# Optimization experiments

Measured on AMD Instinct MI355X. Metric: run time of the kernel, lower is better.

Reference implementation:

```python
import jax, jax.numpy as jnp
import numpy as np
import math

V, D, H, NH, LE, LD = 32000, 256, 1024, 8, 2, 2
B, T = 4, 512


def qlinear(x, W, b):
    # x: [..., Din, 4]; W: [4, Dout, Din] (r,i,j,k); b: [Dout, 4] or None
    r, i, j, k = x[..., 0], x[..., 1], x[..., 2], x[..., 3]
    Wr, Wi, Wj, Wk = W[0], W[1], W[2], W[3]
    f = lambda a, M: jnp.einsum('...d,od->...o', a, M)
    ro = f(r, Wr) - f(i, Wi) - f(j, Wj) - f(k, Wk)
    io = f(r, Wi) + f(i, Wr) + f(j, Wk) - f(k, Wj)
    jo = f(r, Wj) - f(i, Wk) + f(j, Wr) + f(k, Wi)
    ko = f(r, Wk) + f(i, Wj) - f(j, Wi) + f(k, Wr)
    out = jnp.stack([ro, io, jo, ko], axis=-1)
    return out + b if b is not None else out


def modrelu(x, bias):
    # x: [..., F, 4]; bias: [F]
    norm = jnp.linalg.norm(x, axis=-1)
    scale = jax.nn.relu(norm + bias) / (norm + 1e-6)
    return x * scale[..., None]


def qnorm(x, g, beta):
    # normalize each quaternion (last dim of size 4) to unit norm
    n = jnp.sqrt(jnp.sum(x * x, axis=-1, keepdims=True) + 1e-6)
    return g * (x / n) + beta


def qattn(q, k, v, W, b, mask, nh):
    # W: [4(proj q,k,v,out), 4(comp), D, D]; b: [4, D, 4]
    def split(x):
        Bq, Tq, Dq, _ = x.shape
        return x.reshape(Bq, Tq, nh, Dq // nh, 4).transpose(0, 2, 1, 3, 4)
    qh = split(qlinear(q, W[0], b[0]))
    kh = split(qlinear(k, W[1], b[1]))
    vh = split(qlinear(v, W[2], b[2]))
    hd = qh.shape[3]
    s = jnp.einsum('bhqfd,bhkfd->bhqk', qh, kh) / math.sqrt(hd * 4)
    if mask is not None:
        s = jnp.where(mask[:, None] == 0, -jnp.inf, s)
    w = jax.nn.softmax(s, axis=-1)
    o = jnp.einsum('bhqk,bhkfd->bhqfd', w, vh)
    Bq, h, Tq, f, _ = o.shape
    o = o.transpose(0, 2, 1, 3, 4).reshape(Bq, Tq, h * f, 4)
    return qlinear(o, W[3], b[3])


def qff(x, W1, b1, mbias, W2, b2):
    return qlinear(modrelu(qlinear(x, W1, b1), mbias), W2, b2)


def qembed(ids, emb):
    d = emb.shape[-1]
    scale = 1.0 / 10000.0 ** (jnp.arange(d, dtype=jnp.float32) / d)
    r = emb[0][ids]
    i = emb[1][ids] * scale
    j = emb[2][ids] * scale
    k = emb[3][ids] * scale
    n = jnp.sqrt(r * r + i * i + j * j + k * k + 1e-6)
    return jnp.stack([r / n, i / n, j / n, k / n], axis=-1)


def rope(x):
    t, d = x.shape[1], x.shape[2]
    inv = 1.0 / 10000.0 ** (jnp.arange(0, d, 2, dtype=jnp.float32) / d)
    fr = jnp.arange(t, dtype=jnp.float32)[:, None] * inv[None, :]
    ang = jnp.concatenate([jnp.sin(fr), jnp.cos(fr)], axis=-1)  # [T, D]
    return x * ang[None, :, :, None]


def setup_inputs():
    key = jax.random.key(0)
    ks = jax.random.split(key, 12)
    n = lambda k, s: jax.random.normal(k, s, jnp.float32) * 0.02
    src = jax.random.randint(ks[0], (B, T), 0, V)
    tgt = jax.random.randint(ks[1], (B, T), 0, V)
    tgt_mask = jnp.broadcast_to(jnp.tril(jnp.ones((T, T), jnp.int32)), (B, T, T))
    return dict(
        src=src, tgt=tgt, tgt_mask=tgt_mask,
        emb=n(ks[2], (4, V, D)),
        enc_attn_W=n(ks[3], (LE, 4, 4, D, D)), enc_attn_b=jnp.zeros((LE, 4, D, 4)),
        enc_norm_g=jnp.ones((LE, 2, D, 4)), enc_norm_b=jnp.zeros((LE, 2, D, 4)),
        enc_ff_W1=n(ks[4], (LE, 4, H, D)), enc_ff_b1=jnp.zeros((LE, H, 4)),
        enc_ff_mod=jnp.zeros((LE, H)),
        enc_ff_W2=n(ks[5], (LE, 4, D, H)), enc_ff_b2=jnp.zeros((LE, D, 4)),
        dec_sa_W=n(ks[6], (LD, 4, 4, D, D)), dec_sa_b=jnp.zeros((LD, 4, D, 4)),
        dec_ca_W=n(ks[7], (LD, 4, 4, D, D)), dec_ca_b=jnp.zeros((LD, 4, D, 4)),
        dec_norm_g=jnp.ones((LD, 3, D, 4)), dec_norm_b=jnp.zeros((LD, 3, D, 4)),
        dec_ff_W1=n(ks[8], (LD, 4, H, D)), dec_ff_b1=jnp.zeros((LD, H, 4)),
        dec_ff_mod=jnp.zeros((LD, H)),
        dec_ff_W2=n(ks[9], (LD, 4, D, H)), dec_ff_b2=jnp.zeros((LD, D, 4)),
        fc_W=n(ks[10], (V, D)), fc_b=jnp.zeros((V,)),
    )


def reference(src, tgt, tgt_mask, emb,
              enc_attn_W, enc_attn_b, enc_norm_g, enc_norm_b,
              enc_ff_W1, enc_ff_b1, enc_ff_mod, enc_ff_W2, enc_ff_b2,
              dec_sa_W, dec_sa_b, dec_ca_W, dec_ca_b, dec_norm_g, dec_norm_b,
              dec_ff_W1, dec_ff_b1, dec_ff_mod, dec_ff_W2, dec_ff_b2,
              fc_W, fc_b):
    x_src = rope(qembed(src, emb))
    x_tgt = rope(qembed(tgt, emb))
    # encoder stack
    m = x_src
    for l in range(LE):
        m = qnorm(m + qattn(m, m, m, enc_attn_W[l], enc_attn_b[l], None, NH), enc_norm_g[l, 0], enc_norm_b[l, 0])
        m = qnorm(m + qff(m, enc_ff_W1[l], enc_ff_b1[l], enc_ff_mod[l], enc_ff_W2[l], enc_ff_b2[l]), enc_norm_g[l, 1], enc_norm_b[l, 1])
    # decoder stack
    x = x_tgt
    for l in range(LD):
        x = qnorm(x + qattn(x, x, x, dec_sa_W[l], dec_sa_b[l], tgt_mask, NH), dec_norm_g[l, 0], dec_norm_b[l, 0])
        x = qnorm(x + qattn(x, m, m, dec_ca_W[l], dec_ca_b[l], None, NH), dec_norm_g[l, 1], dec_norm_b[l, 1])
        x = qnorm(x + qff(x, dec_ff_W1[l], dec_ff_b1[l], dec_ff_mod[l], dec_ff_W2[l], dec_ff_b2[l]), dec_norm_g[l, 2], dec_norm_b[l, 2])
    real = jnp.linalg.norm(x, axis=-1)  # QuaternionToReal('norm') -> [B, T, D]
    logits = jnp.einsum('btd,vd->btv', real, fc_W) + fc_b
    return logits
```

## Files before the change

### kernel.cpp

```cpp
#include <hip/hip_runtime.h>
#include <math.h>

#define B 4
#define T 512
#define D 256
#define H 1024
#define NH 8
#define V 32000
#define BT (B*T)
#define LE 2
#define LD 2
#define DIM 1024

typedef __attribute__((ext_vector_type(8))) short s16x8;
typedef __attribute__((ext_vector_type(4))) float f32x4;
typedef __attribute__((address_space(3))) void lds_void;
typedef const __attribute__((address_space(1))) void g_void;

__device__ __forceinline__ ushort f2bf(float x) {
  uint u = __float_as_uint(x);
  return (ushort)((u + 0x7fffu + ((u >> 16) & 1u)) >> 16);
}

#define QSCALE 0.08838834764831845f

#define A_CNT  1572864
#define F_CNT  2097152
#define FC_CNT 2048000
#define EMB_CNT (2 * BT * 256)
#define MEGA_TOT (A_CNT + F_CNT + FC_CNT + EMB_CNT)
#define WSTEP  1048576
#define FFW    4194304

__device__ __forceinline__ void qexpand_write(
    const float* __restrict__ src, ushort* __restrict__ dst,
    int o, int d, int Din, int P) {
  float w0 = src[(size_t)o * Din + d];
  float w1 = src[P + (size_t)o * Din + d];
  float w2 = src[2 * (size_t)P + (size_t)o * Din + d];
  float w3 = src[3 * (size_t)P + (size_t)o * Din + d];
  int K4 = Din * 4;
  size_t rbase = (size_t)(o * 4) * K4 + d * 4;
  *(ushort4*)(dst + rbase)          = make_ushort4(f2bf(w0), f2bf(-w1), f2bf(-w2), f2bf(-w3));
  *(ushort4*)(dst + rbase + K4)     = make_ushort4(f2bf(w1), f2bf(w0),  f2bf(w3),  f2bf(-w2));
  *(ushort4*)(dst + rbase + 2 * K4) = make_ushort4(f2bf(w2), f2bf(-w3), f2bf(w0),  f2bf(w1));
  *(ushort4*)(dst + rbase + 3 * K4) = make_ushort4(f2bf(w3), f2bf(w2),  f2bf(-w1), f2bf(w0));
}

__global__ __launch_bounds__(256) void mega_expand_kernel(
    const float* __restrict__ encA, const float* __restrict__ decSA,
    const float* __restrict__ decCA,
    const float* __restrict__ eW1, const float* __restrict__ eW2,
    const float* __restrict__ dW1, const float* __restrict__ dW2,
    const float* __restrict__ fcW,
    ushort* __restrict__ WA, ushort* __restrict__ WF, ushort* __restrict__ Wfc,
    const int* __restrict__ srcIds, const int* __restrict__ tgtIds,
    const float* __restrict__ emb,
    float* __restrict__ xsrc, ushort* __restrict__ xbfs,
    float* __restrict__ xtgt, ushort* __restrict__ xbft) {
  int gid = blockIdx.x * 256 + threadIdx.x;
  if (gid < A_CNT) {
    int u = gid >> 18;
    int p = (gid >> 16) & 3;
    int rem = gid & 65535;
    int o = rem >> 8, d = rem & 255;
    const float* base = (u < 2) ? encA + (size_t)u * 1048576
                      : (u < 4) ? decSA + (size_t)(u - 2) * 1048576
                                : decCA + (size_t)(u - 4) * 1048576;
    qexpand_write(base + (size_t)p * 262144,
                  WA + ((size_t)u * 4 + p) * WSTEP, o, d, 256, 65536);
  } else if (gid < A_CNT + F_CNT) {
    int idx = gid - A_CNT;
    int layer = idx >> 19;
    int w12 = (idx >> 18) & 1;
    int rem = idx & 262143;
    const float* w1b = (layer < 2) ? eW1 + (size_t)layer * 1048576
                                   : dW1 + (size_t)(layer - 2) * 1048576;
    const float* w2b = (layer < 2) ? eW2 + (size_t)layer * 1048576
                                   : dW2 + (size_t)(layer - 2) * 1048576;
    ushort* dst = WF + (size_t)layer * 2 * FFW + (size_t)w12 * FFW;
    if (w12 == 0) {
      int o = rem >> 8, d = rem & 255;
      qexpand_write(w1b, dst, o, d, 256, 262144);
    } else {
      int o = rem >> 10, d = rem & 1023;
      qexpand_write(w2b, dst, o, d, 1024, 262144);
    }
  } else if (gid < A_CNT + F_CNT + FC_CNT) {
    int idx = gid - A_CNT - F_CNT;
    float4 v = ((const float4*)fcW)[idx];
    ((ushort4*)Wfc)[idx] = make_ushort4(f2bf(v.x), f2bf(v.y), f2bf(v.z), f2bf(v.w));
  } else if (gid < MEGA_TOT) {
    int idx = gid - A_CNT - F_CNT - FC_CNT;
    int g = idx >> 8, d = idx & 255;
    int isTgt = g >= BT;
    int bt = isTgt ? g - BT : g;
    int id = isTgt ? tgtIds[bt] : srcIds[bt];
    float* out = isTgt ? xtgt : xsrc;
    ushort* outbf = isTgt ? xbft : xbfs;
    int t = bt % T;
    size_t VD = (size_t)V * D;
    float scale = powf(10000.f, -(float)d / (float)D);
    float r = emb[(size_t)id * D + d];
    float i = emb[VD + (size_t)id * D + d] * scale;
    float j = emb[2 * VD + (size_t)id * D + d] * scale;
    float k = emb[3 * VD + (size_t)id * D + d] * scale;
    float n = sqrtf(r * r + i * i + j * j + k * k + 1e-6f);
    float ang;
    if (d < D / 2) {
      float inv = powf(10000.f, -(float)(2 * d) / (float)D);
      ang = sinf((float)t * inv);
    } else {
      float inv = powf(10000.f, -(float)(2 * (d - D / 2)) / (float)D);
      ang = cosf((float)t * inv);
    }
    float s = ang / n;
    size_t base = (size_t)bt * DIM + d * 4;
    float4 q = make_float4(r * s, i * s, j * s, k * s);
    *(float4*)(out + base) = q;
    *(ushort4*)(outbf + base) = make_ushort4(f2bf(q.x), f2bf(q.y), f2bf(q.z), f2bf(q.w));
  }
}

struct GP {
  const ushort* A; const ushort* Aalt; int altStart;
  const ushort* Bt; const float* bias; void* Cv;
  ushort* qo; ushort* ko; ushort* vo;
  float* xres; ushort* xbf; const float* gg; const float* bb;
  const float* modb; ushort* realout;
};

template <int OMODE, int TM>
__global__ __launch_bounds__(256, 4) void gemm_bf16_kernel(
    GP u0, GP u1, int nunits, int N, int K) {
  constexpr int NBUF = (TM == 64) ? 4 : 2;
  __shared__ ushort As[NBUF][TM * 32];
  __shared__ ushort Bs[NBUF][128 * 32];
  const int tid = threadIdx.x;
  const int w = tid >> 6, l = tid & 63;
  const int nwg = gridDim.x;
  const int qq = nwg >> 3, rr = nwg & 7;
  const int xcd = blockIdx.x & 7, pos = blockIdx.x >> 3;
  const int wg = (xcd < rr ? xcd * (qq + 1) : rr * (qq + 1) + (xcd - rr) * qq) + pos;
  const int uwg = nwg / nunits;
  const int unit = wg / uwg;
  const int wgl = wg - unit * uwg;
  GP U = unit ? u1 : u0;
  const int nbx = N >> 7;
  const int nby = uwg / nbx;
  const int m0 = (wgl % nby) * TM, n0 = (wgl / nby) * 128;
  const ushort* Ap = (U.altStart && n0 >= U.altStart) ? U.Aalt : U.A;
  const ushort* Btp = U.Bt;
  const int lr = l & 15, lg = l >> 4;
  constexpr int NR = (TM == 128) ? 4 : 2;
  const int wm = (TM == 128) ? (w >> 1) : 0;
  const int wn = (TM == 128) ? (w & 1) : w;
  const int wcol = wn * (NR * 16);
  f32x4 acc[4][NR] = {};
  const int NT = K >> 5;

  auto stage = [&](int t, int buf) {
    int k0 = t << 5;
#pragma unroll
    for (int s = 0; s < TM / 64; ++s) {
      int fb = (w * (TM / 64) + s) * 1024;
      int f = fb + l * 16;
      int row = f >> 6, cb = (f & 63) >> 1;
      __builtin_amdgcn_global_load_lds(
          (g_void*)(Ap + (size_t)(m0 + row) * K + k0 + cb),
          (lds_void*)((char*)&As[buf][0] + fb), 16, 0, 0);
    }
#pragma unroll
    for (int s = 0; s < 2; ++s) {
      int fb = (w * 2 + s) * 1024;
      int f = fb + l * 16;
      int row = f >> 6, cb = (f & 63) >> 1;
      __builtin_amdgcn_global_load_lds(
          (g_void*)(Btp + (size_t)(n0 + row) * K + k0 + cb),
          (lds_void*)((char*)&Bs[buf][0] + fb), 16, 0, 0);
    }
  };
  auto compute = [&](int buf) {
    s16x8 af[4], bfr[NR];
#pragma unroll
    for (int mi = 0; mi < 4; ++mi)
      af[mi] = *(const s16x8*)(&As[buf][0] + (wm * 64 + mi * 16 + lr) * 32 + lg * 8);
#pragma unroll
    for (int ni = 0; ni < NR; ++ni)
      bfr[ni] = *(const s16x8*)(&Bs[buf][0] + (wcol + ni * 16 + lr) * 32 + lg * 8);
    __builtin_amdgcn_s_setprio(1);
#pragma unroll
    for (int mi = 0; mi < 4; ++mi)
#pragma unroll
      for (int ni = 0; ni < NR; ++ni)
        acc[mi][ni] = __builtin_amdgcn_mfma_f32_16x16x32_bf16(af[mi], bfr[ni], acc[mi][ni], 0, 0, 0);
    __builtin_amdgcn_s_setprio(0);
  };

  if constexpr (TM == 64) {
    stage(0, 0);
    stage(1, 1);
    __syncthreads();
    for (int t = 0; t < NT; t += 2) {
      if (t + 2 < NT) {
        stage(t + 2, (t + 2) & 3);
        stage(t + 3, (t + 3) & 3);
      }
      compute(t & 3);
      compute((t + 1) & 3);
      __syncthreads();
    }
  } else {
    stage(0, 0);
    __syncthreads();
    int cur = 0;
    for (int t = 0; t < NT; ++t) {
      if (t + 1 < NT) stage(t + 1, cur ^ 1);
      compute(cur);
      __syncthreads();
      cur ^= 1;
    }
  }

#pragma unroll
  for (int mi = 0; mi < 4; ++mi) {
#pragma unroll
    for (int ni = 0; ni < NR; ++ni) {
      int row = m0 + wm * 64 + mi * 16 + lg * 4;
      int col = n0 + wcol + ni * 16 + lr;
      f32x4 v = acc[mi][ni];
      if constexpr (OMODE == 0) {
        float bv = U.bias ? U.bias[col] : 0.f;
        float* C = (float*)U.Cv;
#pragma unroll
        for (int r = 0; r < 4; ++r)
          C[(size_t)(row + r) * N + col] = v[r] + bv;
      } else if constexpr (OMODE == 3) {
        float bv = U.bias[col];
        if (col < 2048) {
          ushort* dst = (col < DIM) ? U.qo : U.ko;
          float sc = (col < DIM) ? QSCALE : 1.f;
          int c = col & (DIM - 1);
#pragma unroll
          for (int r = 0; r < 4; ++r)
            dst[(size_t)(row + r) * DIM + c] = f2bf((v[r] + bv) * sc);
        } else {
          int c = col - 2048;
          ushort4 o4 = make_ushort4(f2bf(v[0] + bv), f2bf(v[1] + bv),
                                    f2bf(v[2] + bv), f2bf(v[3] + bv));
          *(ushort4*)&U.vo[((size_t)((row >> 9) << 10) + c) * T + (row & 511)] = o4;
        }
      } else if constexpr (OMODE == 4) {
        float bv = U.bias[col];
        float gv = U.gg[col], bev = U.bb[col];
#pragma unroll
        for (int r = 0; r < 4; ++r) {
          float val = v[r] + bv + U.xres[(size_t)(row + r) * DIM + col];
          float sq = val * val;
          sq += __shfl_xor(sq, 1);
          sq += __shfl_xor(sq, 2);
          float invn = rsqrtf(sq + 1e-6f);
          float res = gv * (val * invn) + bev;
          U.xres[(size_t)(row + r) * DIM + col] = res;
          U.xbf[(size_t)(row + r) * DIM + col] = f2bf(res);
          if (U.realout) {
            float rsq = res * res;
            rsq += __shfl_xor(rsq, 1);
            rsq += __shfl_xor(rsq, 2);
            if ((col & 3) == 0)
              U.realout[(size_t)(row + r) * D + (col >> 2)] = f2bf(sqrtf(rsq));
          }
        }
      } else {
        float bv = U.bias[col];
        float mb = U.modb[col >> 2];
        ushort* C = (ushort*)U.Cv;
#pragma unroll
        for (int r = 0; r < 4; ++r) {
          float val = v[r] + bv;
          float sq = val * val;
          sq += __shfl_xor(sq, 1);
          sq += __shfl_xor(sq, 2);
          float norm = sqrtf(sq);
          float scale = fmaxf(norm + mb, 0.f) / (norm + 1e-6f);
          C[(size_t)(row + r) * N + col] = f2bf(val * scale);
        }
      }
    }
  }
}

__global__ __launch_bounds__(256) void fused_attn_kernel(
    const ushort* __restrict__ qb, const ushort* __restrict__ kb,
    const ushort* __restrict__ vT, ushort* __restrict__ outA,
    int c0, int c1) {
  __shared__ ushort Ks[2][64 * 128];
  __shared__ ushort Vs[2][128 * 64];
  __shared__ ushort Pst[4][1024];
  const int tid = threadIdx.x;
  const int wq = tid >> 6, l = tid & 63;
  const int lr = l & 15, lg = l >> 4;
  const int h = blockIdx.y;
  const int u = blockIdx.z >> 2, b = blockIdx.z & 3;
  const size_t uoff = (size_t)u * ((size_t)BT * DIM);
  const int causal = u ? c1 : c0;
  const int q0 = blockIdx.x * 64 + wq * 16;
  const size_t bT = (size_t)b * T;
  const int hc = h * 128;
  const size_t vrow0 = (size_t)(b * NH + h) * 128;
  const ushort* qbu = qb + uoff;
  const ushort* kbu = kb + uoff;
  const ushort* vTu = vT + uoff;
  ushort* outu = outA + uoff;
  s16x8 qf[4];
#pragma unroll
  for (int ks = 0; ks < 4; ++ks)
    qf[ks] = *(const s16x8*)(qbu + (bT + q0 + lr) * DIM + hc + ks * 32 + lg * 8);
  f32x4 O[8] = {};
  float m[4] = {-3e38f, -3e38f, -3e38f, -3e38f};
  float lac[4] = {0.f, 0.f, 0.f, 0.f};
  const int kend = causal ? (blockIdx.x + 1) * 64 : T;
  const int ntile = kend >> 6;

  auto stageKV = [&](int tile, int buf) {
    int kv0 = tile << 6;
#pragma unroll
    for (int s = 0; s < 4; ++s) {
      int f = s * 4096 + tid * 16;
      int row = f >> 8, g = (f >> 4) & 15;
      int gs = g ^ (row & 7);
      __builtin_amdgcn_global_load_lds(
          (g_void*)(kbu + (bT + kv0 + row) * DIM + hc + gs * 8),
          (lds_void*)((char*)&Ks[buf][0] + f), 16, 0, 0);
    }
#pragma unroll
    for (int s = 0; s < 4; ++s) {
      int f = s * 4096 + tid * 16;
      int row = f >> 7, g = (f >> 4) & 7;
      int gs = g ^ (row & 7);
      __builtin_amdgcn_global_load_lds(
          (g_void*)(vTu + (vrow0 + row) * T + kv0 + gs * 8),
          (lds_void*)((char*)&Vs[buf][0] + f), 16, 0, 0);
    }
  };

  stageKV(0, 0);
  __syncthreads();
  int cur = 0;
  for (int tile = 0; tile < ntile; ++tile) {
    const int kv0 = tile << 6;
    if (tile + 1 < ntile) stageKV(tile + 1, cur ^ 1);
    f32x4 s[4] = {};
#pragma unroll
    for (int ks = 0; ks < 4; ++ks) {
      s16x8 kf[4];
#pragma unroll
      for (int ni = 0; ni < 4; ++ni) {
        int row = ni * 16 + lr;
        int g = (ks * 4 + lg) ^ (row & 7);
        kf[ni] = *(const s16x8*)(&Ks[cur][0] + row * 128 + g * 8);
      }
#pragma unroll
      for (int ni = 0; ni < 4; ++ni)
        s[ni] = __builtin_amdgcn_mfma_f32_16x16x32_bf16(qf[ks], kf[ni], s[ni], 0, 0, 0);
    }
    const bool domask = causal && (kv0 + 63 > q0);
#pragma unroll
    for (int r = 0; r < 4; ++r) {
      const int qrow = q0 + lg * 4 + r;
      float mx = -3e38f;
#pragma unroll
      for (int ni = 0; ni < 4; ++ni) {
        float v = s[ni][r];
        if (domask && (kv0 + ni * 16 + lr > qrow)) v = -3e38f;
        s[ni][r] = v;
        mx = fmaxf(mx, v);
      }
#pragma unroll
      for (int dd = 1; dd < 16; dd <<= 1) mx = fmaxf(mx, __shfl_xor(mx, dd));
      if (__ballot(mx > m[r] + 8.f)) {
        float mn = fmaxf(m[r], mx);
        float alpha = __expf(m[r] - mn);
        m[r] = mn;
        lac[r] *= alpha;
#pragma unroll
        for (int dni = 0; dni < 8; ++dni) O[dni][r] *= alpha;
      }
      float ps = 0.f;
#pragma unroll
      for (int ni = 0; ni < 4; ++ni) {
        float p = __expf(s[ni][r] - m[r]);
        s[ni][r] = p;
        ps += p;
      }
#pragma unroll
      for (int dd = 1; dd < 16; dd <<= 1) ps += __shfl_xor(ps, dd);
      lac[r] += ps;
      const int qloc = lg * 4 + r;
      const int sw = (qloc & 7) << 3;
#pragma unroll
      for (int ni = 0; ni < 4; ++ni)
        Pst[wq][qloc * 64 + ((ni * 16 + lr) ^ sw)] = f2bf(s[ni][r]);
    }
    asm volatile("s_waitcnt lgkmcnt(0)" ::: "memory");
    __builtin_amdgcn_sched_barrier(0);
#pragma unroll
    for (int ks2 = 0; ks2 < 2; ++ks2) {
      s16x8 pa = *(const s16x8*)&Pst[wq][lr * 64 + ((ks2 * 32 + lg * 8) ^ ((lr & 7) << 3))];
#pragma unroll
      for (int dni = 0; dni < 8; ++dni) {
        int row = dni * 16 + lr;
        int g = (ks2 * 4 + lg) ^ (row & 7);
        s16x8 vf = *(const s16x8*)(&Vs[cur][0] + row * 64 + g * 8);
        O[dni] = __builtin_amdgcn_mfma_f32_16x16x32_bf16(pa, vf, O[dni], 0, 0, 0);
      }
    }
    __syncthreads();
    cur ^= 1;
  }
#pragma unroll
  for (int r = 0; r < 4; ++r) {
    float inv = 1.f / lac[r];
    const size_t row = bT + q0 + lg * 4 + r;
#pragma unroll
    for (int dni = 0; dni < 8; ++dni)
      outu[row * DIM + hc + dni * 16 + lr] = f2bf(O[dni][r] * inv);
  }
}

extern "C" void kernel_launch(void* const* d_in, const int* in_sizes, int n_in,
                              void* d_out, int out_size, void* d_ws, size_t ws_size,
                              hipStream_t stream) {
  const int*   src        = (const int*)d_in[0];
  const int*   tgt        = (const int*)d_in[1];
  const float* emb        = (const float*)d_in[3];
  const float* enc_attn_W = (const float*)d_in[4];
  const float* enc_attn_b = (const float*)d_in[5];
  const float* enc_norm_g = (const float*)d_in[6];
  const float* enc_norm_b = (const float*)d_in[7];
  const float* enc_ff_W1  = (const float*)d_in[8];
  const float* enc_ff_b1  = (const float*)d_in[9];
  const float* enc_ff_mod = (const float*)d_in[10];
  const float* enc_ff_W2  = (const float*)d_in[11];
  const float* enc_ff_b2  = (const float*)d_in[12];
  const float* dec_sa_W   = (const float*)d_in[13];
  const float* dec_sa_b   = (const float*)d_in[14];
  const float* dec_ca_W   = (const float*)d_in[15];
  const float* dec_ca_b   = (const float*)d_in[16];
  const float* dec_norm_g = (const float*)d_in[17];
  const float* dec_norm_b = (const float*)d_in[18];
  const float* dec_ff_W1  = (const float*)d_in[19];
  const float* dec_ff_b1  = (const float*)d_in[20];
  const float* dec_ff_mod = (const float*)d_in[21];
  const float* dec_ff_W2  = (const float*)d_in[22];
  const float* dec_ff_b2  = (const float*)d_in[23];
  const float* fc_W       = (const float*)d_in[24];
  const float* fc_b       = (const float*)d_in[25];
  float* out = (float*)d_out;

  const size_t USZ = (size_t)BT * DIM;
  float* ws    = (float*)d_ws;
  float* xsrc  = ws;
  float* xtgt  = xsrc + USZ;
  ushort* xbf_src = (ushort*)(xtgt + USZ);
  ushort* xbf_tgt = xbf_src + USZ;
  ushort* aobf    = xbf_tgt + USZ;
  ushort* qb      = aobf + 2 * USZ;
  ushort* kb      = qb + 2 * USZ;
  ushort* vTb     = kb + 2 * USZ;
  ushort* hbf     = vTb + 2 * USZ;
  ushort* realbf  = hbf + (size_t)BT * H * 4;
  ushort* WA      = realbf + (size_t)BT * D;
  ushort* WF      = WA + (size_t)6 * 4 * WSTEP;
  ushort* Wfc     = WF + (size_t)4 * 2 * FFW;

  mega_expand_kernel<<<(MEGA_TOT + 255) / 256, 256, 0, stream>>>(
      enc_attn_W, dec_sa_W, dec_ca_W,
      enc_ff_W1, enc_ff_W2, dec_ff_W1, dec_ff_W2, fc_W, WA, WF, Wfc,
      src, tgt, emb, xsrc, xbf_src, xtgt, xbf_tgt);

  GP Z{};

  auto mkQKV = [&](const ushort* Abf, const ushort* Wu, const float* bb, int u) {
    GP g = Z;
    g.A = Abf; g.Bt = Wu; g.bias = bb;
    g.qo = qb + u * USZ; g.ko = kb + u * USZ; g.vo = vTb + u * USZ;
    return g;
  };
  auto mkOP = [&](int u, const ushort* Wu3, const float* bb, float* xres,
                  ushort* xbf, const float* gg, const float* nb, ushort* realo) {
    GP g = Z;
    g.A = aobf + u * USZ; g.Bt = Wu3; g.bias = bb;
    g.xres = xres; g.xbf = xbf; g.gg = gg; g.bb = nb; g.realout = realo;
    return g;
  };

  auto qkv1 = [&](GP g) {
    gemm_bf16_kernel<3, 128><<<384, 256, 0, stream>>>(g, g, 1, 3 * DIM, DIM);
  };
  auto qkv2 = [&](GP g0, GP g1) {
    gemm_bf16_kernel<3, 128><<<768, 256, 0, stream>>>(g0, g1, 2, 3 * DIM, DIM);
  };
  auto op1 = [&](GP g) {
    gemm_bf16_kernel<4, 64><<<256, 256, 0, stream>>>(g, g, 1, DIM, DIM);
  };
  auto op2 = [&](GP g0, GP g1) {
    gemm_bf16_kernel<4, 64><<<512, 256, 0, stream>>>(g0, g1, 2, DIM, DIM);
  };
  auto attn1 = [&](int causal) {
    fused_attn_kernel<<<dim3(T / 64, NH, B), 256, 0, stream>>>(
        qb, kb, vTb, aobf, causal, causal);
  };
  auto ffpair = [&](const ushort* xbf, int layer, const float* b1,
                    const float* mod, const float* b2, float* xres,
                    ushort* xbfo, const float* gg, const float* nb,
                    ushort* realo) {
    const ushort* Wf = WF + (size_t)layer * 2 * FFW;
    GP g1 = Z;
    g1.A = xbf; g1.Bt = Wf; g1.bias = b1; g1.Cv = hbf; g1.modb = mod;
    gemm_bf16_kernel<5, 128><<<512, 256, 0, stream>>>(g1, g1, 1, 4 * H, DIM);
    GP g2 = Z;
    g2.A = hbf; g2.Bt = Wf + FFW; g2.bias = b2;
    g2.xres = xres; g2.xbf = xbfo; g2.gg = gg; g2.bb = nb; g2.realout = realo;
    gemm_bf16_kernel<4, 64><<<256, 256, 0, stream>>>(g2, g2, 1, DIM, 4 * H);
  };

  {
    GP e = mkQKV(xbf_src, WA + (size_t)(0 * 4) * WSTEP, enc_attn_b, 0);
    GP d = mkQKV(xbf_tgt, WA + (size_t)(2 * 4) * WSTEP, dec_sa_b, 1);
    qkv2(e, d);
    fused_attn_kernel<<<dim3(T / 64, NH, 2 * B), 256, 0, stream>>>(
        qb, kb, vTb, aobf, 0, 1);
    GP eo = mkOP(0, WA + (size_t)(0 * 4 + 3) * WSTEP, enc_attn_b + 3 * DIM,
                 xsrc, xbf_src, enc_norm_g, enc_norm_b, nullptr);
    GP dd = mkOP(1, WA + (size_t)(2 * 4 + 3) * WSTEP, dec_sa_b + 3 * DIM,
                 xtgt, xbf_tgt, dec_norm_g, dec_norm_b, nullptr);
    op2(eo, dd);
  }
  ffpair(xbf_src, 0, enc_ff_b1, enc_ff_mod, enc_ff_b2, xsrc, xbf_src,
         enc_norm_g + 1 * DIM, enc_norm_b + 1 * DIM, nullptr);
  {
    GP e = mkQKV(xbf_src, WA + (size_t)(1 * 4) * WSTEP,
                 enc_attn_b + (size_t)1 * 4 * DIM, 0);
    qkv1(e);
    attn1(0);
    GP eo = mkOP(0, WA + (size_t)(1 * 4 + 3) * WSTEP,
                 enc_attn_b + (size_t)1 * 4 * DIM + 3 * DIM,
                 xsrc, xbf_src, enc_norm_g + 2 * DIM, enc_norm_b + 2 * DIM, nullptr);
    op1(eo);
  }
  ffpair(xbf_src, 1, enc_ff_b1 + (size_t)1 * H * 4, enc_ff_mod + H,
         enc_ff_b2 + DIM, xsrc, xbf_src,
         enc_norm_g + 3 * DIM, enc_norm_b + 3 * DIM, nullptr);

  for (int l = 0; l < LD; ++l) {
    if (l > 0) {
      GP d = mkQKV(xbf_tgt, WA + (size_t)((2 + l) * 4) * WSTEP,
                   dec_sa_b + (size_t)l * 4 * DIM, 0);
      qkv1(d);
      attn1(1);
      GP od = mkOP(0, WA + (size_t)((2 + l) * 4 + 3) * WSTEP,
                   dec_sa_b + (size_t)l * 4 * DIM + 3 * DIM,
                   xtgt, xbf_tgt, dec_norm_g + (size_t)(l * 3) * DIM,
                   dec_norm_b + (size_t)(l * 3) * DIM, nullptr);
      op1(od);
    }
    {
      GP g = mkQKV(xbf_tgt, WA + (size_t)((4 + l) * 4) * WSTEP,
                   dec_ca_b + (size_t)l * 4 * DIM, 0);
      g.Aalt = xbf_src; g.altStart = DIM;
      qkv1(g);
      attn1(0);
      GP og = mkOP(0, WA + (size_t)((4 + l) * 4 + 3) * WSTEP,
                   dec_ca_b + (size_t)l * 4 * DIM + 3 * DIM,
                   xtgt, xbf_tgt, dec_norm_g + (size_t)(l * 3 + 1) * DIM,
                   dec_norm_b + (size_t)(l * 3 + 1) * DIM, nullptr);
      op1(og);
    }
    ffpair(xbf_tgt, 2 + l, dec_ff_b1 + (size_t)l * H * 4,
           dec_ff_mod + (size_t)l * H, dec_ff_b2 + (size_t)l * DIM,
           xtgt, xbf_tgt, dec_norm_g + (size_t)(l * 3 + 2) * DIM,
           dec_norm_b + (size_t)(l * 3 + 2) * DIM,
           (l == LD - 1) ? realbf : nullptr);
  }

  {
    GP g = Z;
    g.A = realbf; g.Bt = Wfc; g.bias = fc_b; g.Cv = out;
    gemm_bf16_kernel<0, 128><<<(V / 128) * (BT / 128), 256, 0, stream>>>(
        g, g, 1, V, 256);
  }
}
```

Before: 1.092 ms.

## Split-K the FF2 GEMM into four partials with a separate merge kernel

The second feed-forward GEMM (K=4096, N=1024) now runs as a 4-way split-K launch with 1024 workgroups instead of 256. Each split writes bf16 partial sums to a workspace buffer. A new merge kernel sums the partials and applies the bias, residual add, quaternion norm and the optional real-norm output. The aim is better CU occupancy for the long-K GEMM, paid for with an extra kernel launch, extra partial-sum traffic, and some precision loss from rounding partials to bf16.

```diff
diff --git a/kernel.cpp b/kernel.cpp
--- a/kernel.cpp
+++ b/kernel.cpp
@@ -20,6 +20,9 @@
 __device__ __forceinline__ ushort f2bf(float x) {
   uint u = __float_as_uint(x);
   return (ushort)((u + 0x7fffu + ((u >> 16) & 1u)) >> 16);
+}
+__device__ __forceinline__ float bf2f(ushort u) {
+  return __uint_as_float(((uint)u) << 16);
 }
 
 #define QSCALE 0.08838834764831845f
@@ -130,10 +133,9 @@
   const float* modb; ushort* realout;
 };
 
-template <int OMODE, int TM>
+template <int OMODE, int TM, int NBUF>
 __global__ __launch_bounds__(256, 4) void gemm_bf16_kernel(
-    GP u0, GP u1, int nunits, int N, int K) {
-  constexpr int NBUF = (TM == 64) ? 4 : 2;
+    GP u0, GP u1, int nunits, int nsplit, int N, int K) {
   __shared__ ushort As[NBUF][TM * 32];
   __shared__ ushort Bs[NBUF][128 * 32];
   const int tid = threadIdx.x;
@@ -142,10 +144,14 @@
   const int qq = nwg >> 3, rr = nwg & 7;
   const int xcd = blockIdx.x & 7, pos = blockIdx.x >> 3;
   const int wg = (xcd < rr ? xcd * (qq + 1) : rr * (qq + 1) + (xcd - rr) * qq) + pos;
-  const int uwg = nwg / nunits;
-  const int unit = wg / uwg;
-  const int wgl = wg - unit * uwg;
+  const int uwg = nwg / (nunits * nsplit);
+  const int idx = wg / uwg;
+  const int unit = idx / nsplit;
+  const int split = idx % nsplit;
+  const int wgl = wg % uwg;
   GP U = unit ? u1 : u0;
+  const int Ksub = K / nsplit;
+  const int kbase = split * Ksub;
   const int nbx = N >> 7;
   const int nby = uwg / nbx;
   const int m0 = (wgl % nby) * TM, n0 = (wgl / nby) * 128;
@@ -157,10 +163,10 @@
   const int wn = (TM == 128) ? (w & 1) : w;
   const int wcol = wn * (NR * 16);
   f32x4 acc[4][NR] = {};
-  const int NT = K >> 5;
+  const int NT = Ksub >> 5;
 
   auto stage = [&](int t, int buf) {
-    int k0 = t << 5;
+    int k0 = kbase + (t << 5);
 #pragma unroll
     for (int s = 0; s < TM / 64; ++s) {
       int fb = (w * (TM / 64) + s) * 1024;
@@ -197,7 +203,7 @@
     __builtin_amdgcn_s_setprio(0);
   };
 
-  if constexpr (TM == 64) {
+  if constexpr (NBUF == 4) {
     stage(0, 0);
     stage(1, 1);
     __syncthreads();
@@ -271,7 +277,7 @@
               U.realout[(size_t)(row + r) * D + (col >> 2)] = f2bf(sqrtf(rsq));
           }
         }
-      } else {
+      } else if constexpr (OMODE == 5) {
         float bv = U.bias[col];
         float mb = U.modb[col >> 2];
         ushort* C = (ushort*)U.Cv;
@@ -285,9 +291,46 @@
           float scale = fmaxf(norm + mb, 0.f) / (norm + 1e-6f);
           C[(size_t)(row + r) * N + col] = f2bf(val * scale);
         }
+      } else {
+        ushort* P = (ushort*)U.Cv + (size_t)split * BT * N;
+#pragma unroll
+        for (int r = 0; r < 4; ++r)
+          P[(size_t)(row + r) * N + col] = f2bf(v[r]);
       }
     }
   }
+}
+
+__global__ __launch_bounds__(256) void ff2_merge_kernel(
+    const ushort* __restrict__ P, const float* __restrict__ bias,
+    float* __restrict__ xres, ushort* __restrict__ xbf,
+    const float* __restrict__ gg, const float* __restrict__ bb,
+    ushort* __restrict__ realo) {
+  int idx = blockIdx.x * 256 + threadIdx.x;
+  int row = idx >> 8;
+  int c4 = (idx & 255) << 2;
+  size_t base = (size_t)row * DIM + c4;
+  float a0 = 0.f, a1 = 0.f, a2 = 0.f, a3 = 0.f;
+#pragma unroll
+  for (int sp = 0; sp < 4; ++sp) {
+    ushort4 p = *(const ushort4*)(P + (size_t)sp * BT * DIM + base);
+    a0 += bf2f(p.x); a1 += bf2f(p.y); a2 += bf2f(p.z); a3 += bf2f(p.w);
+  }
+  float4 xv = *(float4*)(xres + base);
+  float v0 = a0 + bias[c4 + 0] + xv.x;
+  float v1 = a1 + bias[c4 + 1] + xv.y;
+  float v2 = a2 + bias[c4 + 2] + xv.z;
+  float v3 = a3 + bias[c4 + 3] + xv.w;
+  float invn = rsqrtf(v0 * v0 + v1 * v1 + v2 * v2 + v3 * v3 + 1e-6f);
+  float r0 = gg[c4 + 0] * (v0 * invn) + bb[c4 + 0];
+  float r1 = gg[c4 + 1] * (v1 * invn) + bb[c4 + 1];
+  float r2 = gg[c4 + 2] * (v2 * invn) + bb[c4 + 2];
+  float r3 = gg[c4 + 3] * (v3 * invn) + bb[c4 + 3];
+  *(float4*)(xres + base) = make_float4(r0, r1, r2, r3);
+  *(ushort4*)(xbf + base) = make_ushort4(f2bf(r0), f2bf(r1), f2bf(r2), f2bf(r3));
+  if (realo)
+    realo[(size_t)row * D + (c4 >> 2)] =
+        f2bf(sqrtf(r0 * r0 + r1 * r1 + r2 * r2 + r3 * r3));
 }
 
 __global__ __launch_bounds__(256) void fused_attn_kernel(
@@ -473,6 +516,7 @@
   ushort* WA      = realbf + (size_t)BT * D;
   ushort* WF      = WA + (size_t)6 * 4 * WSTEP;
   ushort* Wfc     = WF + (size_t)4 * 2 * FFW;
+  ushort* Pff     = Wfc + (size_t)V * D;
 
   mega_expand_kernel<<<(MEGA_TOT + 255) / 256, 256, 0, stream>>>(
       enc_attn_W, dec_sa_W, dec_ca_W,
@@ -496,16 +540,16 @@
   };
 
   auto qkv1 = [&](GP g) {
-    gemm_bf16_kernel<3, 128><<<384, 256, 0, stream>>>(g, g, 1, 3 * DIM, DIM);
+    gemm_bf16_kernel<3, 128, 2><<<384, 256, 0, stream>>>(g, g, 1, 1, 3 * DIM, DIM);
   };
   auto qkv2 = [&](GP g0, GP g1) {
-    gemm_bf16_kernel<3, 128><<<768, 256, 0, stream>>>(g0, g1, 2, 3 * DIM, DIM);
+    gemm_bf16_kernel<3, 128, 2><<<768, 256, 0, stream>>>(g0, g1, 2, 1, 3 * DIM, DIM);
   };
   auto op1 = [&](GP g) {
-    gemm_bf16_kernel<4, 64><<<256, 256, 0, stream>>>(g, g, 1, DIM, DIM);
+    gemm_bf16_kernel<4, 64, 4><<<256, 256, 0, stream>>>(g, g, 1, 1, DIM, DIM);
   };
   auto op2 = [&](GP g0, GP g1) {
-    gemm_bf16_kernel<4, 64><<<512, 256, 0, stream>>>(g0, g1, 2, DIM, DIM);
+    gemm_bf16_kernel<4, 64, 4><<<512, 256, 0, stream>>>(g0, g1, 2, 1, DIM, DIM);
   };
   auto attn1 = [&](int causal) {
     fused_attn_kernel<<<dim3(T / 64, NH, B), 256, 0, stream>>>(
@@ -518,11 +562,11 @@
     const ushort* Wf = WF + (size_t)layer * 2 * FFW;
     GP g1 = Z;
     g1.A = xbf; g1.Bt = Wf; g1.bias = b1; g1.Cv = hbf; g1.modb = mod;
-    gemm_bf16_kernel<5, 128><<<512, 256, 0, stream>>>(g1, g1, 1, 4 * H, DIM);
+    gemm_bf16_kernel<5, 128, 2><<<512, 256, 0, stream>>>(g1, g1, 1, 1, 4 * H, DIM);
     GP g2 = Z;
-    g2.A = hbf; g2.Bt = Wf + FFW; g2.bias = b2;
-    g2.xres = xres; g2.xbf = xbfo; g2.gg = gg; g2.bb = nb; g2.realout = realo;
-    gemm_bf16_kernel<4, 64><<<256, 256, 0, stream>>>(g2, g2, 1, DIM, 4 * H);
+    g2.A = hbf; g2.Bt = Wf + FFW; g2.Cv = Pff;
+    gemm_bf16_kernel<6, 64, 2><<<1024, 256, 0, stream>>>(g2, g2, 1, 4, DIM, 4 * H);
+    ff2_merge_kernel<<<BT, 256, 0, stream>>>(Pff, b2, xres, xbfo, gg, nb, realo);
   };
 
   {
@@ -587,7 +631,7 @@
   {
     GP g = Z;
     g.A = realbf; g.Bt = Wfc; g.bias = fc_b; g.Cv = out;
-    gemm_bf16_kernel<0, 128><<<(V / 128) * (BT / 128), 256, 0, stream>>>(
-        g, g, 1, V, 256);
-  }
-}
+    gemm_bf16_kernel<0, 128, 2><<<(V / 128) * (BT / 128), 256, 0, stream>>>(
+        g, g, 1, 1, V, 256);
+  }
+}
```

Measured after the change: 961.7 us. 11.9% less time.
